# Kernel optimization log

Hardware: AMD Instinct MI355X
Metric: run time of the kernel (lower is better)

Reference implementation:

```python
import jax, jax.numpy as jnp
import numpy as np

B, L, D = 4096, 50, 128          # users, neighbors/user, embed_dim
N_U, N_I, N_R, N_T = 10000, 100000, 6, 1000
EPS = 1e-5                       # BatchNorm eps (eval mode, running stats)


def setup_inputs() -> dict:
    key = jax.random.key(0)
    ks = iter(jax.random.split(key, 80))
    nk = lambda: next(ks)

    def lin(din, dout):
        s = 1.0 / np.sqrt(din)
        w = jax.random.uniform(nk(), (din, dout), minval=-s, maxval=s, dtype=jnp.float32)
        b = jax.random.uniform(nk(), (dout,), minval=-s, maxval=s, dtype=jnp.float32)
        return w, b

    inp = {}
    # embedding tables (u2e/i2e/r2e/t2e)
    inp['u2e'] = 0.1 * jax.random.normal(nk(), (N_U, D), jnp.float32)
    inp['i2e'] = 0.1 * jax.random.normal(nk(), (N_I, D), jnp.float32)
    inp['r2e'] = 0.1 * jax.random.normal(nk(), (N_R, D), jnp.float32)
    inp['t2e'] = 0.1 * jax.random.normal(nk(), (N_T, D), jnp.float32)
    # neighbor transform MLP
    inp['ne_w'], inp['ne_b'] = lin(3 * D, D)
    inp['ne1_w'], inp['ne1_b'] = lin(D, D)
    # attention MLP (NewAttention: concat(neigh, user) -> D -> D -> 1, softmax over neighbors)
    inp['att1_w'], inp['att1_b'] = lin(2 * D, D)
    inp['att2_w'], inp['att2_b'] = lin(D, D)
    inp['att3_w'], inp['att3_b'] = lin(D, 1)
    # head
    inp['lin_w'], inp['lin_b'] = lin(2 * D, D)
    inp['w1_w'], inp['w1_b'] = lin(D, D // 4)
    inp['bn1_g'] = jnp.ones((D // 4,), jnp.float32)
    inp['bn1_b'] = jnp.zeros((D // 4,), jnp.float32)
    inp['bn1_m'] = 0.1 * jax.random.normal(nk(), (D // 4,), jnp.float32)
    inp['bn1_v'] = jax.random.uniform(nk(), (D // 4,), minval=0.5, maxval=1.5, dtype=jnp.float32)
    inp['w2_w'], inp['w2_b'] = lin(D // 4, D // 8)
    inp['bn2_g'] = jnp.ones((D // 8,), jnp.float32)
    inp['bn2_b'] = jnp.zeros((D // 8,), jnp.float32)
    inp['bn2_m'] = 0.1 * jax.random.normal(nk(), (D // 8,), jnp.float32)
    inp['bn2_v'] = jax.random.uniform(nk(), (D // 8,), minval=0.5, maxval=1.5, dtype=jnp.float32)
    inp['w3_w'], inp['w3_b'] = lin(D // 8, 1)
    # index inputs (padded-fixed neighbor lists)
    inp['user_idx'] = jax.random.randint(nk(), (B,), 0, N_U)
    inp['item_idx'] = jax.random.randint(nk(), (B, L), 0, N_I)
    inp['rat_idx'] = jax.random.randint(nk(), (B, L), 0, N_R)
    inp['time_idx'] = jax.random.randint(nk(), (B, L), 0, N_T)
    return inp


def reference(u2e, i2e, r2e, t2e, ne_w, ne_b, ne1_w, ne1_b,
              att1_w, att1_b, att2_w, att2_b, att3_w, att3_b,
              lin_w, lin_b, w1_w, w1_b, bn1_g, bn1_b, bn1_m, bn1_v,
              w2_w, w2_b, bn2_g, bn2_b, bn2_m, bn2_v, w3_w, w3_b,
              user_idx, item_idx, rat_idx, time_idx):
    u = u2e[user_idx]                                                   # [B, D]
    neigh = jnp.concatenate([i2e[item_idx], r2e[rat_idx], t2e[time_idx]], axis=-1)  # [B, L, 3D]
    x = jax.nn.relu(neigh @ ne_w + ne_b)                                # [B, L, D]
    x = jax.nn.relu(x @ ne1_w + ne1_b)                                  # [B, L, D]
    # attention over neighbors, conditioned on the user embedding
    a = jnp.concatenate([x, jnp.broadcast_to(u[:, None, :], x.shape)], axis=-1)  # [B, L, 2D]
    a = jax.nn.relu(a @ att1_w + att1_b)
    a = jax.nn.relu(a @ att2_w + att2_b)
    att = jax.nn.softmax((a @ att3_w + att3_b)[..., 0], axis=-1)        # [B, L]
    pooled = jnp.einsum('bl,bld->bd', att, x)                           # torch.mm(x.t(), att).t()
    comb = jax.nn.relu(jnp.concatenate([u, pooled], axis=-1) @ lin_w + lin_b)  # [B, D]
    h = comb @ w1_w + w1_b
    h = jax.nn.relu((h - bn1_m) * jax.lax.rsqrt(bn1_v + EPS) * bn1_g + bn1_b)
    h = h @ w2_w + w2_b
    h = jax.nn.relu((h - bn2_m) * jax.lax.rsqrt(bn2_v + EPS) * bn2_g + bn2_b)
    return (h @ w3_w + w3_b)[:, 0]                                      # [B]
```

## Files before the change

### kernel.cpp

```cpp
#include <hip/hip_runtime.h>
#include <hip/hip_bf16.h>

typedef __bf16 bf16x8 __attribute__((ext_vector_type(8)));
typedef float  f32x4  __attribute__((ext_vector_type(4)));

#define W_OFF 0
#define A_OFF 32768
#define X_OFF 46080
#define SMALL 59392
#define SMEM_TOTAL 63488
#define WCHUNK 16384

#define WS_WPREP 0
#define WS_PI    262144
#define WS_PT    (WS_PI + 51200000)
#define WS_PR    (WS_PT + 512000)
#define WS_PU    (WS_PR + 3072)
#define WS_PU2   (WS_PU + 5120000)

__global__ void prep_weights_kernel(const float* __restrict__ ne_w,
                                    const float* __restrict__ ne1_w,
                                    const float* __restrict__ att1_w,
                                    const float* __restrict__ att2_w,
                                    const float* __restrict__ lin_w,
                                    __hip_bfloat16* __restrict__ wout) {
  __shared__ float tile[64][65];
  const int bx = blockIdx.x;
  const int c = bx >> 2, kt = (bx >> 1) & 1, ntile = bx & 1;
  const float* src; int koff;
  if      (c < 3)  { src = ne_w;   koff = c * 128; }
  else if (c == 3) { src = ne1_w;  koff = 0; }
  else if (c == 4) { src = att1_w; koff = 0; }
  else if (c == 5) { src = att2_w; koff = 0; }
  else if (c == 6) { src = att1_w; koff = 128; }
  else             { src = lin_w;  koff = 0; }
  const int tx = threadIdx.x, ty = threadIdx.y;
#pragma unroll
  for (int r = 0; r < 16; ++r) {
    int k = kt * 64 + r * 4 + ty, n = ntile * 64 + tx;
    tile[r * 4 + ty][tx] = src[(koff + k) * 128 + n];
  }
  __syncthreads();
#pragma unroll
  for (int r = 0; r < 16; ++r) {
    int n = ntile * 64 + r * 4 + ty, k = kt * 64 + tx;
    int off = (c * 128 + n) * 128 + (((k >> 3) ^ (n & 15)) << 3) + (k & 7);
    wout[off] = __float2bfloat16(tile[tx][r * 4 + ty]);
  }
}

__device__ __forceinline__ unsigned short bf_bits(float x) {
  return __builtin_bit_cast(unsigned short, __float2bfloat16(x));
}

__device__ __forceinline__ void mfma_chunk(const __hip_bfloat16* sIn,
                                           const __hip_bfloat16* sWl,
                                           f32x4 acc[4], int m16, int nh, int lane) {
  const int mr = lane & 15;
  const int kq = lane >> 4;
  const int arow = (m16 * 16 + mr) * 128;
#pragma unroll
  for (int ks = 0; ks < 4; ++ks) {
    const int swz = (((ks * 4 + kq) ^ mr) << 3);
    bf16x8 a = *(const bf16x8*)(sIn + arow + swz);
#pragma unroll
    for (int nt = 0; nt < 4; ++nt) {
      const int n = nh * 64 + nt * 16 + mr;
      bf16x8 b = *(const bf16x8*)(sWl + n * 128 + swz);
      acc[nt] = __builtin_amdgcn_mfma_f32_16x16x32_bf16(a, b, acc[nt], 0, 0, 0);
    }
  }
}

__device__ __forceinline__ void epilogue(f32x4 acc[4], const float* __restrict__ bias,
                                         const float* addvec, __hip_bfloat16* sOut,
                                         int m16, int nh, int lane) {
  const int mr = lane & 15;
  const int rb = m16 * 16 + ((lane >> 4) << 2);
#pragma unroll
  for (int nt = 0; nt < 4; ++nt) {
    const int col = nh * 64 + nt * 16 + mr;
    float bv = bias[col];
    if (addvec) bv += addvec[col];
    const int cblk = col >> 3, clo = col & 7;
#pragma unroll
    for (int r = 0; r < 4; ++r) {
      const int row = rb + r;
      if (row < 50) {
        float v = fmaxf(acc[nt][r] + bv, 0.0f);
        sOut[row * 128 + ((cblk ^ (row & 15)) << 3) + clo] = __float2bfloat16(v);
      }
    }
  }
}

__global__ __launch_bounds__(512) void pgemm_kernel(
    const float* __restrict__ i2e, const float* __restrict__ r2e,
    const float* __restrict__ t2e, const float* __restrict__ u2e,
    const float* __restrict__ ne_b, const __hip_bfloat16* __restrict__ wprep,
    float* __restrict__ Pi, float* __restrict__ Pt, float* __restrict__ Pr,
    float* __restrict__ Pu, float* __restrict__ Pu2) {
  __shared__ __align__(16) __hip_bfloat16 sW[WCHUNK];
  __shared__ __align__(16) __hip_bfloat16 sA[64 * 128];
  const int tid = threadIdx.x, lane = tid & 63, wid = tid >> 6;
  const int m16 = wid & 3, nh = wid >> 2;
  const int bx = blockIdx.x;
  const float* src; const __hip_bfloat16* W; float* dst; const float* addb = nullptr;
  long rows0; int nrows;
  if (bx < 1563)      { src = i2e; W = wprep + 0 * WCHUNK; dst = Pi;  rows0 = (long)bx * 64;          nrows = 100000; }
  else if (bx < 1579) { src = t2e; W = wprep + 2 * WCHUNK; dst = Pt;  rows0 = (long)(bx - 1563) * 64; nrows = 1000; }
  else if (bx < 1580) { src = r2e; W = wprep + 1 * WCHUNK; dst = Pr;  rows0 = 0;                      nrows = 6; addb = ne_b; }
  else if (bx < 1737) { src = u2e; W = wprep + 6 * WCHUNK; dst = Pu;  rows0 = (long)(bx - 1580) * 64; nrows = 10000; }
  else                { src = u2e; W = wprep + 7 * WCHUNK; dst = Pu2; rows0 = (long)(bx - 1737) * 64; nrows = 10000; }

#pragma unroll
  for (int i = 0; i < 4; ++i) {
    int g = tid + i * 512;
    __builtin_amdgcn_global_load_lds(
        (__attribute__((address_space(1))) void*)(void*)(W + g * 8),
        (__attribute__((address_space(3))) void*)(void*)(sW + g * 8), 16, 0, 0);
  }
  const float4* s4 = (const float4*)src;
#pragma unroll
  for (int i = 0; i < 2; ++i) {
    int g = tid + i * 512;
    int row = g >> 4, kb = g & 15;
    float4 v0 = {0.f, 0.f, 0.f, 0.f}, v1 = {0.f, 0.f, 0.f, 0.f};
    if (rows0 + row < nrows) {
      long base = (rows0 + row) * 32 + kb * 2;
      v0 = s4[base]; v1 = s4[base + 1];
    }
    uint4 pk;
    pk.x = ((unsigned)bf_bits(v0.y) << 16) | bf_bits(v0.x);
    pk.y = ((unsigned)bf_bits(v0.w) << 16) | bf_bits(v0.z);
    pk.z = ((unsigned)bf_bits(v1.y) << 16) | bf_bits(v1.x);
    pk.w = ((unsigned)bf_bits(v1.w) << 16) | bf_bits(v1.z);
    *(uint4*)(sA + row * 128 + ((kb ^ (row & 15)) << 3)) = pk;
  }
  __syncthreads();

  f32x4 acc[4];
#pragma unroll
  for (int j = 0; j < 4; ++j) acc[j] = (f32x4){0.f, 0.f, 0.f, 0.f};
  mfma_chunk(sA, sW, acc, m16, nh, lane);

  const int mr = lane & 15;
  const int rb = m16 * 16 + ((lane >> 4) << 2);
#pragma unroll
  for (int nt = 0; nt < 4; ++nt) {
    const int col = nh * 64 + nt * 16 + mr;
    const float bv = addb ? addb[col] : 0.f;
#pragma unroll
    for (int r = 0; r < 4; ++r) {
      const int row = rb + r;
      if (rows0 + row < nrows) dst[(rows0 + row) * 128 + col] = acc[nt][r] + bv;
    }
  }
}

__global__ __launch_bounds__(512, 4) void graphdec_main(
    const float* __restrict__ Pi, const float* __restrict__ Pt,
    const float* __restrict__ Pr, const float* __restrict__ Pu,
    const float* __restrict__ Pu2,
    const float* __restrict__ ne1_b, const float* __restrict__ att1_b,
    const float* __restrict__ att2_b, const float* __restrict__ att3_w,
    const float* __restrict__ lin_w, const float* __restrict__ lin_b,
    const float* __restrict__ w1_w, const float* __restrict__ w1_b,
    const float* __restrict__ bn1_g, const float* __restrict__ bn1_b,
    const float* __restrict__ bn1_m, const float* __restrict__ bn1_v,
    const float* __restrict__ w2_w, const float* __restrict__ w2_b,
    const float* __restrict__ bn2_g, const float* __restrict__ bn2_b,
    const float* __restrict__ bn2_m, const float* __restrict__ bn2_v,
    const float* __restrict__ w3_w, const float* __restrict__ w3_b,
    const int* __restrict__ user_idx, const int* __restrict__ item_idx,
    const int* __restrict__ rat_idx, const int* __restrict__ time_idx,
    const __hip_bfloat16* __restrict__ wprep, float* __restrict__ out) {
  __shared__ __align__(16) unsigned char smem[SMEM_TOTAL];
  __hip_bfloat16* sW = (__hip_bfloat16*)(smem + W_OFF);
  __hip_bfloat16* sA = (__hip_bfloat16*)(smem + A_OFF);
  __hip_bfloat16* sX = (__hip_bfloat16*)(smem + X_OFF);
  int*   sIdx   = (int*)  (smem + SMALL);
  float* sUatt  = (float*)(smem + SMALL + 768);
  float* sUlin  = (float*)(smem + SMALL + 1280);
  float* sLP0   = (float*)(smem + SMALL + 1792);
  float* sLP1   = (float*)(smem + SMALL + 2048);
  float* sAtt   = (float*)(smem + SMALL + 2304);
  float* sPooled= (float*)(smem + SMALL + 2560);
  float* sComb  = (float*)(smem + SMALL + 3072);
  float* sH1    = (float*)(smem + SMALL + 3584);
  float* sPool4 = (float*)(smem + W_OFF);
  float* sCombP = (float*)(smem + W_OFF + 2048);

  const int tid  = threadIdx.x;
  const int lane = tid & 63;
  const int wid  = tid >> 6;
  const int m16  = wid & 3;
  const int nh   = wid >> 2;
  const int b    = blockIdx.x;

  float att3r[4];
#pragma unroll
  for (int nt = 0; nt < 4; ++nt) att3r[nt] = att3_w[nh * 64 + nt * 16 + (lane & 15)];

  if (tid < 192) {
    int c = tid >> 6, l = tid & 63;
    int v = 0;
    if (l < 50) {
      const int* p = (c == 0) ? item_idx : (c == 1) ? rat_idx : time_idx;
      v = p[b * 50 + l];
    }
    sIdx[tid] = v;
  }
  const int uid = user_idx[b];
  if (tid >= 256 && tid < 384)      sUatt[tid - 256] = Pu [(long)uid * 128 + (tid - 256)];
  else if (tid >= 384)              sUlin[tid - 384] = Pu2[(long)uid * 128 + (tid - 384)];
  __syncthreads();

  auto stage = [&](const __hip_bfloat16* __restrict__ src) {
#pragma unroll
    for (int i = 0; i < 4; ++i) {
      int g = tid + i * 512;
      __builtin_amdgcn_global_load_lds(
          (__attribute__((address_space(1))) void*)(void*)(src + g * 8),
          (__attribute__((address_space(3))) void*)(void*)(sW + g * 8), 16, 0, 0);
    }
  };

  f32x4 acc[4];
  const f32x4 zf = {0.f, 0.f, 0.f, 0.f};
  auto zacc = [&]() {
#pragma unroll
    for (int j = 0; j < 4; ++j) acc[j] = zf;
  };

  stage(wprep + 3 * WCHUNK);
#pragma unroll
  for (int i = 0; i < 2; ++i) {
    int g = tid + i * 512;
    if (g < 832) {
      int row = g >> 4, kb = g & 15;
      uint4 pk = {0u, 0u, 0u, 0u};
      if (row < 50) {
        const float4* pi4 = (const float4*)(Pi + (long)sIdx[row] * 128) + kb * 2;
        const float4* pr4 = (const float4*)(Pr + (long)sIdx[64 + row] * 128) + kb * 2;
        const float4* pt4 = (const float4*)(Pt + (long)sIdx[128 + row] * 128) + kb * 2;
        float4 a0 = pi4[0], a1 = pi4[1];
        float4 r0 = pr4[0], r1 = pr4[1];
        float4 t0 = pt4[0], t1 = pt4[1];
        float s0 = fmaxf(a0.x + r0.x + t0.x, 0.f);
        float s1 = fmaxf(a0.y + r0.y + t0.y, 0.f);
        float s2 = fmaxf(a0.z + r0.z + t0.z, 0.f);
        float s3 = fmaxf(a0.w + r0.w + t0.w, 0.f);
        float s4 = fmaxf(a1.x + r1.x + t1.x, 0.f);
        float s5 = fmaxf(a1.y + r1.y + t1.y, 0.f);
        float s6 = fmaxf(a1.z + r1.z + t1.z, 0.f);
        float s7 = fmaxf(a1.w + r1.w + t1.w, 0.f);
        pk.x = ((unsigned)bf_bits(s1) << 16) | bf_bits(s0);
        pk.y = ((unsigned)bf_bits(s3) << 16) | bf_bits(s2);
        pk.z = ((unsigned)bf_bits(s5) << 16) | bf_bits(s4);
        pk.w = ((unsigned)bf_bits(s7) << 16) | bf_bits(s6);
      }
      *(uint4*)(sA + row * 128 + ((kb ^ (row & 15)) << 3)) = pk;
    }
  }
  __syncthreads();

  zacc();
  mfma_chunk(sA, sW, acc, m16, nh, lane);
  __syncthreads();
  stage(wprep + 4 * WCHUNK);
  epilogue(acc, ne1_b, nullptr, sX, m16, nh, lane);
  __syncthreads();

  zacc();
  mfma_chunk(sX, sW, acc, m16, nh, lane);
  __syncthreads();
  stage(wprep + 5 * WCHUNK);
  epilogue(acc, att1_b, sUatt, sA, m16, nh, lane);
  __syncthreads();

  zacc();
  mfma_chunk(sA, sW, acc, m16, nh, lane);
  {
    float lp[4] = {0.f, 0.f, 0.f, 0.f};
#pragma unroll
    for (int nt = 0; nt < 4; ++nt) {
      const int col = nh * 64 + nt * 16 + (lane & 15);
      const float b2 = att2_b[col];
#pragma unroll
      for (int r = 0; r < 4; ++r)
        lp[r] += fmaxf(acc[nt][r] + b2, 0.f) * att3r[nt];
    }
#pragma unroll
    for (int off = 1; off < 16; off <<= 1) {
#pragma unroll
      for (int r = 0; r < 4; ++r) lp[r] += __shfl_xor(lp[r], off);
    }
    if ((lane & 15) == 0) {
      const int rowb = m16 * 16 + ((lane >> 4) << 2);
      float* dst = nh ? sLP1 : sLP0;
#pragma unroll
      for (int r = 0; r < 4; ++r) dst[rowb + r] = lp[r];
    }
  }
  __syncthreads();

  if (wid == 0) {
    float v = (lane < 50) ? (sLP0[lane] + sLP1[lane]) : -3.4e38f;
    float m = v;
    for (int off = 32; off > 0; off >>= 1) m = fmaxf(m, __shfl_xor(m, off));
    float e = (lane < 50) ? __expf(v - m) : 0.f;
    float s = e;
    for (int off = 32; off > 0; off >>= 1) s += __shfl_xor(s, off);
    sAtt[lane] = e / s;
  }
  __syncthreads();

  {
    int q = tid >> 7, d = tid & 127;
    const int cblk = d >> 3, clo = d & 7;
    float s = 0.f;
    for (int l = q; l < 50; l += 4)
      s += sAtt[l] * (float)sX[l * 128 + ((cblk ^ (l & 15)) << 3) + clo];
    sPool4[q * 128 + d] = s;
  }
  __syncthreads();
  if (tid < 128)
    sPooled[tid] = sPool4[tid] + sPool4[128 + tid] + sPool4[256 + tid] + sPool4[384 + tid];
  __syncthreads();

  {
    int q = tid >> 7, d = tid & 127;
    float s = 0.f;
    for (int j = q * 32; j < q * 32 + 32; ++j) s += sPooled[j] * lin_w[(128 + j) * 128 + d];
    sCombP[q * 128 + d] = s;
  }
  __syncthreads();
  if (tid < 128)
    sComb[tid] = fmaxf(sCombP[tid] + sCombP[128 + tid] + sCombP[256 + tid] + sCombP[384 + tid]
                       + sUlin[tid] + lin_b[tid], 0.f);
  __syncthreads();

  if (wid == 0) {
    if (lane < 32) {
      float s = w1_b[lane];
      for (int k = 0; k < 128; ++k) s += sComb[k] * w1_w[k * 32 + lane];
      s = (s - bn1_m[lane]) * rsqrtf(bn1_v[lane] + 1e-5f) * bn1_g[lane] + bn1_b[lane];
      sH1[lane] = fmaxf(s, 0.f);
    }
    if (lane < 16) {
      float s = w2_b[lane];
      for (int k = 0; k < 32; ++k) s += sH1[k] * w2_w[k * 16 + lane];
      s = (s - bn2_m[lane]) * rsqrtf(bn2_v[lane] + 1e-5f) * bn2_g[lane] + bn2_b[lane];
      float p = fmaxf(s, 0.f) * w3_w[lane];
      p += __shfl_xor(p, 1); p += __shfl_xor(p, 2);
      p += __shfl_xor(p, 4); p += __shfl_xor(p, 8);
      if (lane == 0) out[b] = p + w3_b[0];
    }
  }
}

extern "C" void kernel_launch(void* const* d_in, const int* in_sizes, int n_in,
                              void* d_out, int out_size, void* d_ws, size_t ws_size,
                              hipStream_t stream) {
  const float* u2e    = (const float*)d_in[0];
  const float* i2e    = (const float*)d_in[1];
  const float* r2e    = (const float*)d_in[2];
  const float* t2e    = (const float*)d_in[3];
  const float* ne_w   = (const float*)d_in[4];
  const float* ne_b   = (const float*)d_in[5];
  const float* ne1_w  = (const float*)d_in[6];
  const float* ne1_b  = (const float*)d_in[7];
  const float* att1_w = (const float*)d_in[8];
  const float* att1_b = (const float*)d_in[9];
  const float* att2_w = (const float*)d_in[10];
  const float* att2_b = (const float*)d_in[11];
  const float* att3_w = (const float*)d_in[12];
  const float* att3_b = (const float*)d_in[13];
  const float* lin_w  = (const float*)d_in[14];
  const float* lin_b  = (const float*)d_in[15];
  const float* w1_w   = (const float*)d_in[16];
  const float* w1_b   = (const float*)d_in[17];
  const float* bn1_g  = (const float*)d_in[18];
  const float* bn1_b  = (const float*)d_in[19];
  const float* bn1_m  = (const float*)d_in[20];
  const float* bn1_v  = (const float*)d_in[21];
  const float* w2_w   = (const float*)d_in[22];
  const float* w2_b   = (const float*)d_in[23];
  const float* bn2_g  = (const float*)d_in[24];
  const float* bn2_b  = (const float*)d_in[25];
  const float* bn2_m  = (const float*)d_in[26];
  const float* bn2_v  = (const float*)d_in[27];
  const float* w3_w   = (const float*)d_in[28];
  const float* w3_b   = (const float*)d_in[29];
  const int* user_idx = (const int*)d_in[30];
  const int* item_idx = (const int*)d_in[31];
  const int* rat_idx  = (const int*)d_in[32];
  const int* time_idx = (const int*)d_in[33];
  (void)att3_b;

  char* ws = (char*)d_ws;
  __hip_bfloat16* wprep = (__hip_bfloat16*)(ws + WS_WPREP);
  float* Pi  = (float*)(ws + WS_PI);
  float* Pt  = (float*)(ws + WS_PT);
  float* Pr  = (float*)(ws + WS_PR);
  float* Pu  = (float*)(ws + WS_PU);
  float* Pu2 = (float*)(ws + WS_PU2);
  float* out = (float*)d_out;

  prep_weights_kernel<<<32, dim3(64, 4), 0, stream>>>(ne_w, ne1_w, att1_w, att2_w,
                                                      lin_w, wprep);
  pgemm_kernel<<<1894, 512, 0, stream>>>(i2e, r2e, t2e, u2e, ne_b, wprep,
                                         Pi, Pt, Pr, Pu, Pu2);
  graphdec_main<<<4096, 512, 0, stream>>>(
      Pi, Pt, Pr, Pu, Pu2, ne1_b, att1_b, att2_b, att3_w,
      lin_w, lin_b, w1_w, w1_b, bn1_g, bn1_b, bn1_m, bn1_v, w2_w, w2_b,
      bn2_g, bn2_b, bn2_m, bn2_v, w3_w, w3_b,
      user_idx, item_idx, rat_idx, time_idx, wprep, out);
}
```

Baseline: 269.2 us.

## Store item projections as bf16 and stage weights in K-halves to raise occupancy

The precomputed item projection table Pi is now written and read in bf16 instead of fp32, halving the projection write and the per-neighbor gather traffic. Weight tiles are re-laid out in two 64-wide K halves so the main kernel keeps only half a weight matrix in LDS, cutting shared memory per block and raising the launch-bounds occupancy hint from 4 to 6. The cost is extra barriers and a second staging pass per layer, plus an added bf16 rounding on the item projection before the bias add.

```diff
diff --git a/kernel.cpp b/kernel.cpp
--- a/kernel.cpp
+++ b/kernel.cpp
@@ -5,15 +5,16 @@
 typedef float  f32x4  __attribute__((ext_vector_type(4)));
 
 #define W_OFF 0
-#define A_OFF 32768
-#define X_OFF 46080
-#define SMALL 59392
-#define SMEM_TOTAL 63488
+#define A_OFF 16384
+#define X_OFF 29696
+#define SMALL 43008
+#define SMEM_TOTAL 47104
 #define WCHUNK 16384
+#define WHALF  8192
 
 #define WS_WPREP 0
 #define WS_PI    262144
-#define WS_PT    (WS_PI + 51200000)
+#define WS_PT    (WS_PI + 25600000)
 #define WS_PR    (WS_PT + 512000)
 #define WS_PU    (WS_PR + 3072)
 #define WS_PU2   (WS_PU + 5120000)
@@ -44,7 +45,8 @@
 #pragma unroll
   for (int r = 0; r < 16; ++r) {
     int n = ntile * 64 + r * 4 + ty, k = kt * 64 + tx;
-    int off = (c * 128 + n) * 128 + (((k >> 3) ^ (n & 15)) << 3) + (k & 7);
+    int h = k >> 6, k64 = k & 63;
+    int off = c * WCHUNK + h * WHALF + n * 64 + ((((k64 >> 3) ^ (n & 7))) << 3) + (k64 & 7);
     wout[off] = __float2bfloat16(tile[tx][r * 4 + ty]);
   }
 }
@@ -53,20 +55,21 @@
   return __builtin_bit_cast(unsigned short, __float2bfloat16(x));
 }
 
-__device__ __forceinline__ void mfma_chunk(const __hip_bfloat16* sIn,
-                                           const __hip_bfloat16* sWl,
-                                           f32x4 acc[4], int m16, int nh, int lane) {
+__device__ __forceinline__ void mfma_half(const __hip_bfloat16* sIn,
+                                          const __hip_bfloat16* sWh,
+                                          f32x4 acc[4], int h, int m16, int nh, int lane) {
   const int mr = lane & 15;
   const int kq = lane >> 4;
   const int arow = (m16 * 16 + mr) * 128;
 #pragma unroll
-  for (int ks = 0; ks < 4; ++ks) {
-    const int swz = (((ks * 4 + kq) ^ mr) << 3);
-    bf16x8 a = *(const bf16x8*)(sIn + arow + swz);
+  for (int ks = 0; ks < 2; ++ks) {
+    const int kb16 = h * 8 + ks * 4 + kq;
+    bf16x8 a = *(const bf16x8*)(sIn + arow + ((kb16 ^ mr) << 3));
+    const int swzb = (((ks * 4 + kq) ^ (mr & 7)) << 3);
 #pragma unroll
     for (int nt = 0; nt < 4; ++nt) {
       const int n = nh * 64 + nt * 16 + mr;
-      bf16x8 b = *(const bf16x8*)(sWl + n * 128 + swz);
+      bf16x8 b = *(const bf16x8*)(sWh + n * 64 + swzb);
       acc[nt] = __builtin_amdgcn_mfma_f32_16x16x32_bf16(a, b, acc[nt], 0, 0, 0);
     }
   }
@@ -98,16 +101,17 @@
     const float* __restrict__ i2e, const float* __restrict__ r2e,
     const float* __restrict__ t2e, const float* __restrict__ u2e,
     const float* __restrict__ ne_b, const __hip_bfloat16* __restrict__ wprep,
-    float* __restrict__ Pi, float* __restrict__ Pt, float* __restrict__ Pr,
+    __hip_bfloat16* __restrict__ Pi, float* __restrict__ Pt, float* __restrict__ Pr,
     float* __restrict__ Pu, float* __restrict__ Pu2) {
   __shared__ __align__(16) __hip_bfloat16 sW[WCHUNK];
   __shared__ __align__(16) __hip_bfloat16 sA[64 * 128];
   const int tid = threadIdx.x, lane = tid & 63, wid = tid >> 6;
   const int m16 = wid & 3, nh = wid >> 2;
   const int bx = blockIdx.x;
-  const float* src; const __hip_bfloat16* W; float* dst; const float* addb = nullptr;
+  const float* src; const __hip_bfloat16* W; float* dst = nullptr;
+  const float* addb = nullptr; bool bf_out = false;
   long rows0; int nrows;
-  if (bx < 1563)      { src = i2e; W = wprep + 0 * WCHUNK; dst = Pi;  rows0 = (long)bx * 64;          nrows = 100000; }
+  if (bx < 1563)      { src = i2e; W = wprep + 0 * WCHUNK; bf_out = true; rows0 = (long)bx * 64;          nrows = 100000; }
   else if (bx < 1579) { src = t2e; W = wprep + 2 * WCHUNK; dst = Pt;  rows0 = (long)(bx - 1563) * 64; nrows = 1000; }
   else if (bx < 1580) { src = r2e; W = wprep + 1 * WCHUNK; dst = Pr;  rows0 = 0;                      nrows = 6; addb = ne_b; }
   else if (bx < 1737) { src = u2e; W = wprep + 6 * WCHUNK; dst = Pu;  rows0 = (long)(bx - 1580) * 64; nrows = 10000; }
@@ -142,7 +146,8 @@
   f32x4 acc[4];
 #pragma unroll
   for (int j = 0; j < 4; ++j) acc[j] = (f32x4){0.f, 0.f, 0.f, 0.f};
-  mfma_chunk(sA, sW, acc, m16, nh, lane);
+  mfma_half(sA, sW, acc, 0, m16, nh, lane);
+  mfma_half(sA, sW + WHALF, acc, 1, m16, nh, lane);
 
   const int mr = lane & 15;
   const int rb = m16 * 16 + ((lane >> 4) << 2);
@@ -153,13 +158,16 @@
 #pragma unroll
     for (int r = 0; r < 4; ++r) {
       const int row = rb + r;
-      if (rows0 + row < nrows) dst[(rows0 + row) * 128 + col] = acc[nt][r] + bv;
-    }
-  }
-}
-
-__global__ __launch_bounds__(512, 4) void graphdec_main(
-    const float* __restrict__ Pi, const float* __restrict__ Pt,
+      if (rows0 + row < nrows) {
+        if (bf_out) Pi[(rows0 + row) * 128 + col] = __float2bfloat16(acc[nt][r]);
+        else        dst[(rows0 + row) * 128 + col] = acc[nt][r] + bv;
+      }
+    }
+  }
+}
+
+__global__ __launch_bounds__(512, 6) void graphdec_main(
+    const __hip_bfloat16* __restrict__ Pi, const float* __restrict__ Pt,
     const float* __restrict__ Pr, const float* __restrict__ Pu,
     const float* __restrict__ Pu2,
     const float* __restrict__ ne1_b, const float* __restrict__ att1_b,
@@ -216,9 +224,9 @@
   else if (tid >= 384)              sUlin[tid - 384] = Pu2[(long)uid * 128 + (tid - 384)];
   __syncthreads();
 
-  auto stage = [&](const __hip_bfloat16* __restrict__ src) {
-#pragma unroll
-    for (int i = 0; i < 4; ++i) {
+  auto stage16 = [&](const __hip_bfloat16* __restrict__ src) {
+#pragma unroll
+    for (int i = 0; i < 2; ++i) {
       int g = tid + i * 512;
       __builtin_amdgcn_global_load_lds(
           (__attribute__((address_space(1))) void*)(void*)(src + g * 8),
@@ -233,7 +241,7 @@
     for (int j = 0; j < 4; ++j) acc[j] = zf;
   };
 
-  stage(wprep + 3 * WCHUNK);
+  stage16(wprep + 3 * WCHUNK);
 #pragma unroll
   for (int i = 0; i < 2; ++i) {
     int g = tid + i * 512;
@@ -241,20 +249,19 @@
       int row = g >> 4, kb = g & 15;
       uint4 pk = {0u, 0u, 0u, 0u};
       if (row < 50) {
-        const float4* pi4 = (const float4*)(Pi + (long)sIdx[row] * 128) + kb * 2;
+        const bf16x8 pv = *(const bf16x8*)(Pi + (long)sIdx[row] * 128 + kb * 8);
         const float4* pr4 = (const float4*)(Pr + (long)sIdx[64 + row] * 128) + kb * 2;
         const float4* pt4 = (const float4*)(Pt + (long)sIdx[128 + row] * 128) + kb * 2;
-        float4 a0 = pi4[0], a1 = pi4[1];
         float4 r0 = pr4[0], r1 = pr4[1];
         float4 t0 = pt4[0], t1 = pt4[1];
-        float s0 = fmaxf(a0.x + r0.x + t0.x, 0.f);
-        float s1 = fmaxf(a0.y + r0.y + t0.y, 0.f);
-        float s2 = fmaxf(a0.z + r0.z + t0.z, 0.f);
-        float s3 = fmaxf(a0.w + r0.w + t0.w, 0.f);
-        float s4 = fmaxf(a1.x + r1.x + t1.x, 0.f);
-        float s5 = fmaxf(a1.y + r1.y + t1.y, 0.f);
-        float s6 = fmaxf(a1.z + r1.z + t1.z, 0.f);
-        float s7 = fmaxf(a1.w + r1.w + t1.w, 0.f);
+        float s0 = fmaxf((float)pv[0] + r0.x + t0.x, 0.f);
+        float s1 = fmaxf((float)pv[1] + r0.y + t0.y, 0.f);
+        float s2 = fmaxf((float)pv[2] + r0.z + t0.z, 0.f);
+        float s3 = fmaxf((float)pv[3] + r0.w + t0.w, 0.f);
+        float s4 = fmaxf((float)pv[4] + r1.x + t1.x, 0.f);
+        float s5 = fmaxf((float)pv[5] + r1.y + t1.y, 0.f);
+        float s6 = fmaxf((float)pv[6] + r1.z + t1.z, 0.f);
+        float s7 = fmaxf((float)pv[7] + r1.w + t1.w, 0.f);
         pk.x = ((unsigned)bf_bits(s1) << 16) | bf_bits(s0);
         pk.y = ((unsigned)bf_bits(s3) << 16) | bf_bits(s2);
         pk.z = ((unsigned)bf_bits(s5) << 16) | bf_bits(s4);
@@ -266,21 +273,33 @@
   __syncthreads();
 
   zacc();
-  mfma_chunk(sA, sW, acc, m16, nh, lane);
-  __syncthreads();
-  stage(wprep + 4 * WCHUNK);
+  mfma_half(sA, sW, acc, 0, m16, nh, lane);
+  __syncthreads();
+  stage16(wprep + 3 * WCHUNK + WHALF);
+  __syncthreads();
+  mfma_half(sA, sW, acc, 1, m16, nh, lane);
+  __syncthreads();
+  stage16(wprep + 4 * WCHUNK);
   epilogue(acc, ne1_b, nullptr, sX, m16, nh, lane);
   __syncthreads();
 
   zacc();
-  mfma_chunk(sX, sW, acc, m16, nh, lane);
-  __syncthreads();
-  stage(wprep + 5 * WCHUNK);
+  mfma_half(sX, sW, acc, 0, m16, nh, lane);
+  __syncthreads();
+  stage16(wprep + 4 * WCHUNK + WHALF);
+  __syncthreads();
+  mfma_half(sX, sW, acc, 1, m16, nh, lane);
+  __syncthreads();
+  stage16(wprep + 5 * WCHUNK);
   epilogue(acc, att1_b, sUatt, sA, m16, nh, lane);
   __syncthreads();
 
   zacc();
-  mfma_chunk(sA, sW, acc, m16, nh, lane);
+  mfma_half(sA, sW, acc, 0, m16, nh, lane);
+  __syncthreads();
+  stage16(wprep + 5 * WCHUNK + WHALF);
+  __syncthreads();
+  mfma_half(sA, sW, acc, 1, m16, nh, lane);
   {
     float lp[4] = {0.f, 0.f, 0.f, 0.f};
 #pragma unroll
@@ -401,7 +420,7 @@
 
   char* ws = (char*)d_ws;
   __hip_bfloat16* wprep = (__hip_bfloat16*)(ws + WS_WPREP);
-  float* Pi  = (float*)(ws + WS_PI);
+  __hip_bfloat16* Pi = (__hip_bfloat16*)(ws + WS_PI);
   float* Pt  = (float*)(ws + WS_PT);
   float* Pr  = (float*)(ws + WS_PR);
   float* Pu  = (float*)(ws + WS_PU);
```

Result: faster. 245.0 us (-9.0%).
